# Kernel tuning notes

Hardware: AMD Instinct MI355X
Metric: run time of the kernel (lower is better)

Reference implementation:

```python
import jax, jax.numpy as jnp
import numpy as np

IGNORE_INDEX = -100


def setup_inputs() -> dict:
    key = jax.random.key(0)
    k_e, k_c, k_t = jax.random.split(key, 3)
    B, T, D, V = 1, 8192, 1024, 50257
    e = jax.random.normal(k_e, (B, T, D), dtype=jnp.float32)
    c = jax.random.normal(k_c, (V, D), dtype=jnp.float32) * (D ** -0.5)
    targets = jax.random.randint(k_t, (B, T), 0, V, dtype=jnp.int64)
    bias = jnp.zeros((V,), dtype=jnp.float32)
    return {"e": e, "c": c, "targets": targets, "bias": bias}


def _linear_cross_entropy(e, c, bias, targets, ignore_index=IGNORE_INDEX,
                          softcap=None, reduction="mean"):
    B, T, D = e.shape
    V = c.shape[0]
    ef = e.reshape(B * T, D)
    tf = targets.reshape(B * T)
    # logits: [N, V] = e @ c^T + bias
    logits = jnp.einsum("nd,vd->nv", ef, c) + bias
    if softcap is not None:
        logits = softcap * jnp.tanh(logits / softcap)
    # stable cross entropy: lse - logit[target]
    lse = jax.nn.logsumexp(logits, axis=-1)  # [N]
    safe_t = jnp.where(tf == ignore_index, 0, tf)
    tgt_logit = jnp.take_along_axis(logits, safe_t[:, None], axis=-1)[:, 0]
    nll = lse - tgt_logit  # [N]
    valid = (tf != ignore_index)
    nll = jnp.where(valid, nll, 0.0)
    if reduction == "mean":
        denom = jnp.maximum(valid.sum().astype(nll.dtype), 1.0)
        return nll.sum() / denom
    elif reduction == "sum":
        return nll.sum()
    else:  # 'none'
        return nll.reshape(B, T)


def reference(e, c, targets, bias):
    return _linear_cross_entropy(e, c, bias, targets)
```

## Files before the change

### kernel.cpp

```cpp
#include <hip/hip_runtime.h>
#include <hip/hip_bf16.h>
#include <math.h>


#define BM 128
#define BN 128
#define BKB 128

typedef int   i32x8 __attribute__((ext_vector_type(8)));
typedef float f32x4 __attribute__((ext_vector_type(4)));

__device__ __forceinline__ void load_lds16(const void* g, void* l) {
    __builtin_amdgcn_global_load_lds(
        (const __attribute__((address_space(1))) void*)g,
        (__attribute__((address_space(3))) void*)l, 16, 0, 0);
}

__device__ __forceinline__ unsigned char f2e4m3_sw(float x) {
    unsigned u = __float_as_uint(x);
    unsigned s = (u >> 24) & 0x80;
    float ax = __uint_as_float(u & 0x7fffffff);
    if (ax != ax) return (unsigned char)(s | 0x7f);
    if (ax >= 448.f) return (unsigned char)(s | 0x7e);
    if (ax < 0.0009765625f) return (unsigned char)s;
    if (ax < 0.015625f) {
        int n = (int)rintf(ax * 512.f);
        return (unsigned char)(s | n);
    }
    int e = (int)((u >> 23) & 0xff) - 127;
    unsigned m = u & 0x7fffff;
    unsigned keep = m >> 20, rest = m & 0xfffff;
    if (rest > 0x80000u || (rest == 0x80000u && (keep & 1))) keep++;
    if (keep == 8) { keep = 0; e++; if (e > 8) return (unsigned char)(s | 0x7e); }
    return (unsigned char)(s | ((e + 7) << 3) | keep);
}

__device__ __forceinline__ unsigned int pk4_fp8(float a, float b, float c, float d) {
#if __has_builtin(__builtin_amdgcn_cvt_pk_fp8_f32)
    int v = __builtin_amdgcn_cvt_pk_fp8_f32(a, b, 0, false);
    v = __builtin_amdgcn_cvt_pk_fp8_f32(c, d, v, true);
    return (unsigned int)v;
#else
    return (unsigned int)f2e4m3_sw(a) | ((unsigned int)f2e4m3_sw(b) << 8) |
           ((unsigned int)f2e4m3_sw(c) << 16) | ((unsigned int)f2e4m3_sw(d) << 24);
#endif
}

__global__ void cast_all_fp8(const float* __restrict__ e,
                             const float* __restrict__ c,
                             unsigned char* __restrict__ e_f8,
                             unsigned char* __restrict__ c_f8,
                             long ne, long ncs, long ncd) {
    long i8 = ((long)blockIdx.x * blockDim.x + threadIdx.x) * 8;
    if (i8 >= ne + ncd) return;
    const float* src;
    unsigned char* dst;
    float scale;
    bool zero = false;
    if (i8 < ne) {
        src = e + i8; dst = e_f8 + i8; scale = 1.0f;
    } else {
        long j8 = i8 - ne;
        dst = c_f8 + j8; scale = 16.0f;
        src = c + j8;
        zero = (j8 + 7 >= ncs);
    }
    uint2 o;
    if (!zero) {
        float4 v0 = *(const float4*)(src);
        float4 v1 = *(const float4*)(src + 4);
        o.x = pk4_fp8(v0.x * scale, v0.y * scale, v0.z * scale, v0.w * scale);
        o.y = pk4_fp8(v1.x * scale, v1.y * scale, v1.z * scale, v1.w * scale);
    } else {
        o.x = o.y = 0u;
    }
    *(uint2*)dst = o;
}

__global__ __launch_bounds__(256)
void gemm_lse_partial(const unsigned char* __restrict__ E,
                      const unsigned char* __restrict__ C,
                      const float* __restrict__ bias,
                      const int* __restrict__ targets,
                      float* __restrict__ row_sum,
                      float* __restrict__ tgt,
                      int N, int D, int V) {
    __shared__ unsigned char As[BM * BKB];
    __shared__ unsigned char Bs[BN * BKB];
    __shared__ float bias_s[BN];
    __shared__ int tgt_s[BM];
    __shared__ float red_s[2][BM];

    const int t = threadIdx.x;
    const int w = t >> 6;
    const int l = t & 63;
    const int quad = l >> 4;
    const int lm = l & 15;
    const int wr0 = (w >> 1) * 64;
    const int wc0 = (w & 1) * 64;

    const int mt = blockIdx.x;
    const int vt = blockIdx.y;

    if (t < BN) {
        int col = vt * BN + t;
        bias_s[t] = (col < V) ? bias[col] : -INFINITY;
    }
    if (t >= BN && t < BN + BM)
        tgt_s[t - BN] = targets[mt * BM + (t - BN)];

    const int srow = t >> 3;
    const int schunk = (t & 7) ^ (srow & 7);
    const unsigned char* ga = E + (long)(mt * BM + srow) * D + schunk * 16;
    const unsigned char* gb = C + (long)(vt * BN + srow) * D + schunk * 16;
    char* lA = (char*)As + w * 1024;
    char* lB = (char*)Bs + w * 1024;
    const long rnd = 32L * D;

    f32x4 acc[4][4] = {};
    const int sA = 127;
    const int sB = 123;

    for (int k0 = 0; k0 < D; k0 += BKB) {
#pragma unroll
        for (int ro = 0; ro < 4; ro++) {
            load_lds16(ga + k0 + ro * rnd, lA + ro * 4096);
            load_lds16(gb + k0 + ro * rnd, lB + ro * 4096);
        }
        __syncthreads();

        const int c0 = ((quad << 1) ^ (lm & 7)) << 4;
        const int c1 = c0 ^ 16;
        i32x8 a_frag[4], b_frag[4];
#pragma unroll
        for (int ti = 0; ti < 4; ti++) {
            const unsigned char* pr = As + (wr0 + ti * 16 + lm) * 128;
            int4 lo = *(const int4*)(pr + c0);
            int4 hi = *(const int4*)(pr + c1);
            a_frag[ti] = (i32x8){lo.x, lo.y, lo.z, lo.w, hi.x, hi.y, hi.z, hi.w};
        }
#pragma unroll
        for (int tj = 0; tj < 4; tj++) {
            const unsigned char* pr = Bs + (wc0 + tj * 16 + lm) * 128;
            int4 lo = *(const int4*)(pr + c0);
            int4 hi = *(const int4*)(pr + c1);
            b_frag[tj] = (i32x8){lo.x, lo.y, lo.z, lo.w, hi.x, hi.y, hi.z, hi.w};
        }
#pragma unroll
        for (int ti = 0; ti < 4; ti++)
#pragma unroll
            for (int tj = 0; tj < 4; tj++)
                acc[ti][tj] = __builtin_amdgcn_mfma_scale_f32_16x16x128_f8f6f4(
                    a_frag[ti], b_frag[tj], acc[ti][tj], 0, 0, 0, sA, 0, sB);
        __syncthreads();
    }

    float bvals[4];
#pragma unroll
    for (int tj = 0; tj < 4; tj++) bvals[tj] = bias_s[wc0 + tj * 16 + lm];

#pragma unroll
    for (int ti = 0; ti < 4; ti++) {
#pragma unroll
        for (int r = 0; r < 4; r++) {
            const int row_local = wr0 + ti * 16 + quad * 4 + r;
            const int tl = tgt_s[row_local] - vt * BN;
            float srow_ = 0.f;
#pragma unroll
            for (int tj = 0; tj < 4; tj++) {
                float v = acc[ti][tj][r] + bvals[tj];
                srow_ += __expf(v);
                if (wc0 + tj * 16 + lm == tl)
                    tgt[mt * BM + row_local] = v;
            }
#pragma unroll
            for (int off = 1; off < 16; off <<= 1)
                srow_ += __shfl_xor(srow_, off, 64);
            if (lm == 0)
                red_s[w & 1][row_local] = srow_;
        }
    }
    __syncthreads();
    if (t < BM)
        atomicAdd(&row_sum[(long)mt * BM + t], red_s[0][t] + red_s[1][t]);
}

__global__ void lse_finish(const float* __restrict__ row_sum,
                           const float* __restrict__ tgt,
                           const int* __restrict__ targets,
                           float* __restrict__ gacc, int N) {
    __shared__ float sred[8];
    int r = blockIdx.x * 256 + threadIdx.x;
    float nll = 0.f, cnt = 0.f;
    if (r < N) {
        int tg = targets[r];
        if (tg != -100) { nll = logf(row_sum[r]) - tgt[r]; cnt = 1.f; }
    }
#pragma unroll
    for (int off = 32; off; off >>= 1) {
        nll += __shfl_xor(nll, off, 64);
        cnt += __shfl_xor(cnt, off, 64);
    }
    int w = threadIdx.x >> 6, l = threadIdx.x & 63;
    if (l == 0) { sred[w] = nll; sred[4 + w] = cnt; }
    __syncthreads();
    if (threadIdx.x == 0) {
        atomicAdd(gacc, sred[0] + sred[1] + sred[2] + sred[3]);
        atomicAdd(gacc + 1, sred[4] + sred[5] + sred[6] + sred[7]);
    }
}

__global__ void final_scalar(const float* __restrict__ gacc, float* __restrict__ out) {
    out[0] = gacc[0] / fmaxf(gacc[1], 1.f);
}

extern "C" void kernel_launch(void* const* d_in, const int* in_sizes, int n_in,
                              void* d_out, int out_size, void* d_ws, size_t ws_size,
                              hipStream_t stream) {
    const float* e       = (const float*)d_in[0];
    const float* c       = (const float*)d_in[1];
    const int*   targets = (const int*)d_in[2];
    const float* bias    = (const float*)d_in[3];
    float* out = (float*)d_out;

    const int N = in_sizes[2];
    const int V = in_sizes[3];
    const int D = in_sizes[0] / N;
    const int mtiles = N / BM;
    const int vtiles = (V + BN - 1) / BN;
    const long Vpad = (long)vtiles * BN;

    char* ws = (char*)d_ws;
    size_t off = 0;
    auto alloc = [&](size_t bytes) {
        void* p = ws + off;
        off += (bytes + 255) & ~(size_t)255;
        return p;
    };
    unsigned char* e_f8 = (unsigned char*)alloc((size_t)N * D);
    unsigned char* c_f8 = (unsigned char*)alloc((size_t)Vpad * D);
    float* row_sum = (float*)alloc((size_t)N * 4);
    float* gacc    = (float*)alloc(8);
    float* tgt     = (float*)alloc((size_t)N * 4);

    hipMemsetAsync(row_sum, 0, (size_t)N * 4 + 256 + 8, stream);

    const long ne  = (long)N * D;
    const long ncs = (long)V * D;
    const long ncd = Vpad * D;
    const long tot8 = (ne + ncd) / 8;
    cast_all_fp8<<<(int)((tot8 + 255) / 256), 256, 0, stream>>>(
        e, c, e_f8, c_f8, ne, ncs, ncd);

    dim3 grid(mtiles, vtiles);
    gemm_lse_partial<<<grid, 256, 0, stream>>>(e_f8, c_f8, bias, targets,
                                               row_sum, tgt, N, D, V);

    lse_finish<<<(N + 255) / 256, 256, 0, stream>>>(row_sum, tgt, targets, gacc, N);
    final_scalar<<<1, 1, 0, stream>>>(gacc, out);
}
```

Baseline: 855.0 us.

## Use 256x256 tiles with double-buffered LDS pipeline and grid swizzle

Enlarges the GEMM tile to 256x256 with 512 threads. It double-buffers A and B in 128KB of LDS, issuing the global-to-LDS loads for the next K slice while MFMAs run on the current one, using explicit waitcnt, barriers and setprio. It also remaps block IDs with an XCD-aware swizzle over a 1D grid. The goal is to hide memory latency and raise data reuse per tile, at the cost of heavier register and LDS pressure and strict assumptions about D and the padding of N and V.

New measurement: 3.067 ms. 259% more time.

```diff
diff --git a/kernel.cpp b/kernel.cpp
--- a/kernel.cpp
+++ b/kernel.cpp
@@ -3,8 +3,8 @@
 #include <math.h>
 
 
-#define BM 128
-#define BN 128
+#define BM 256
+#define BN 256
 #define BKB 128
 
 typedef int   i32x8 __attribute__((ext_vector_type(8)));
@@ -77,112 +77,166 @@
     *(uint2*)dst = o;
 }
 
-__global__ __launch_bounds__(256)
+
+#define VM4 asm volatile("s_waitcnt vmcnt(4)" ::: "memory")
+#define VM0 asm volatile("s_waitcnt vmcnt(0)" ::: "memory")
+#define NOPW ((void)0)
+
+#define STG_A(k, h, b) do {                                                   \
+    const unsigned char* _s = gA + (size_t)(h) * 128 * D + (size_t)(k) * 128; \
+    load_lds16(_s,          lA + (b) * 32768 + (h) * 16384);                  \
+    load_lds16(_s + rowD64, lA + (b) * 32768 + (h) * 16384 + 8192);           \
+} while (0)
+
+#define STG_B(k, h, b) do {                                                   \
+    const unsigned char* _s = gB + (size_t)(h) * 128 * D + (size_t)(k) * 128; \
+    load_lds16(_s,          lB + (b) * 32768 + (h) * 16384);                  \
+    load_lds16(_s + rowD64, lB + (b) * 32768 + (h) * 16384 + 8192);           \
+} while (0)
+
+#define LDA_FRAG(dst, ti, b) do {                                             \
+    const unsigned char* _pr = ldsA + (b) * 32768 + (wr0 + (ti) * 16 + lm) * 128; \
+    int4 _lo = *(const int4*)(_pr + c0);                                      \
+    int4 _hi = *(const int4*)(_pr + c1);                                      \
+    dst = (i32x8){_lo.x, _lo.y, _lo.z, _lo.w, _hi.x, _hi.y, _hi.z, _hi.w};    \
+} while (0)
+
+#define LDB_FRAG(dst, tj, b) do {                                             \
+    const unsigned char* _pr = ldsB + (b) * 32768 + (wc0 + (tj) * 16 + lm) * 128; \
+    int4 _lo = *(const int4*)(_pr + c0);                                      \
+    int4 _hi = *(const int4*)(_pr + c1);                                      \
+    dst = (i32x8){_lo.x, _lo.y, _lo.z, _lo.w, _hi.x, _hi.y, _hi.z, _hi.w};    \
+} while (0)
+
+#define MFMA1(a, bfr, c) __builtin_amdgcn_mfma_scale_f32_16x16x128_f8f6f4(    \
+    (a), (bfr), (c), 0, 0, 0, sA, 0, sB)
+
+#define PHASE(q, b, LOADB, STAGE, WAITV) do {                                 \
+    i32x8 _a0, _a1;                                                           \
+    LDA_FRAG(_a0, 2 * (q), b);                                                \
+    LDA_FRAG(_a1, 2 * (q) + 1, b);                                            \
+    if (LOADB) {                                                              \
+        LDB_FRAG(bf0, 0, b); LDB_FRAG(bf1, 1, b);                             \
+        LDB_FRAG(bf2, 2, b); LDB_FRAG(bf3, 3, b);                             \
+    }                                                                         \
+    STAGE;                                                                    \
+    WAITV;                                                                    \
+    __builtin_amdgcn_s_barrier();                                             \
+    asm volatile("s_waitcnt lgkmcnt(0)" ::: "memory");                        \
+    __builtin_amdgcn_sched_barrier(0);                                        \
+    __builtin_amdgcn_s_setprio(1);                                            \
+    acc[2 * (q)][0]     = MFMA1(_a0, bf0, acc[2 * (q)][0]);                   \
+    acc[2 * (q)][1]     = MFMA1(_a0, bf1, acc[2 * (q)][1]);                   \
+    acc[2 * (q)][2]     = MFMA1(_a0, bf2, acc[2 * (q)][2]);                   \
+    acc[2 * (q)][3]     = MFMA1(_a0, bf3, acc[2 * (q)][3]);                   \
+    acc[2 * (q) + 1][0] = MFMA1(_a1, bf0, acc[2 * (q) + 1][0]);               \
+    acc[2 * (q) + 1][1] = MFMA1(_a1, bf1, acc[2 * (q) + 1][1]);               \
+    acc[2 * (q) + 1][2] = MFMA1(_a1, bf2, acc[2 * (q) + 1][2]);               \
+    acc[2 * (q) + 1][3] = MFMA1(_a1, bf3, acc[2 * (q) + 1][3]);               \
+    __builtin_amdgcn_s_setprio(0);                                            \
+    __builtin_amdgcn_sched_barrier(0);                                        \
+    __builtin_amdgcn_s_barrier();                                             \
+    asm volatile("" ::: "memory");                                            \
+} while (0)
+
+__global__ __launch_bounds__(512, 2)
 void gemm_lse_partial(const unsigned char* __restrict__ E,
                       const unsigned char* __restrict__ C,
                       const float* __restrict__ bias,
                       const int* __restrict__ targets,
                       float* __restrict__ row_sum,
                       float* __restrict__ tgt,
-                      int N, int D, int V) {
-    __shared__ unsigned char As[BM * BKB];
-    __shared__ unsigned char Bs[BN * BKB];
-    __shared__ float bias_s[BN];
-    __shared__ int tgt_s[BM];
-    __shared__ float red_s[2][BM];
-
-    const int t = threadIdx.x;
-    const int w = t >> 6;
-    const int l = t & 63;
+                      int N, int D, int V, int mtiles) {
+    __shared__ unsigned char smem[131072];
+    unsigned char* ldsA = smem;
+    unsigned char* ldsB = smem + 65536;
+
+    const int t_ = threadIdx.x;
+    const int w  = t_ >> 6;
+    const int l  = t_ & 63;
     const int quad = l >> 4;
     const int lm = l & 15;
-    const int wr0 = (w >> 1) * 64;
-    const int wc0 = (w & 1) * 64;
-
-    const int mt = blockIdx.x;
-    const int vt = blockIdx.y;
-
-    if (t < BN) {
-        int col = vt * BN + t;
-        bias_s[t] = (col < V) ? bias[col] : -INFINITY;
-    }
-    if (t >= BN && t < BN + BM)
-        tgt_s[t - BN] = targets[mt * BM + (t - BN)];
-
-    const int srow = t >> 3;
-    const int schunk = (t & 7) ^ (srow & 7);
-    const unsigned char* ga = E + (long)(mt * BM + srow) * D + schunk * 16;
-    const unsigned char* gb = C + (long)(vt * BN + srow) * D + schunk * 16;
-    char* lA = (char*)As + w * 1024;
-    char* lB = (char*)Bs + w * 1024;
-    const long rnd = 32L * D;
-
-    f32x4 acc[4][4] = {};
+    const int wr0 = (w >> 2) * 128;
+    const int wc0 = (w & 3) * 64;
+    const int c0 = ((quad << 1) ^ (lm & 7)) << 4;
+    const int c1 = c0 ^ 16;
+
+    const int nwg = (int)gridDim.x;
+    int swz;
+    if (nwg & 7) swz = (int)blockIdx.x;
+    else         swz = ((int)blockIdx.x & 7) * (nwg >> 3) + ((int)blockIdx.x >> 3);
+    const int mt = swz % mtiles;
+    const int vt = swz / mtiles;
+    const int m0 = mt * BM;
+    const int v0 = vt * BN;
+
+    const int sr = t_ >> 3;
+    const int gc = (t_ & 7) ^ (sr & 7);
+    const unsigned char* gA = E + (size_t)(m0 + sr) * D + gc * 16;
+    const unsigned char* gB = C + (size_t)(v0 + sr) * D + gc * 16;
+    unsigned char* lA = ldsA + w * 1024;
+    unsigned char* lB = ldsB + w * 1024;
+    const size_t rowD64 = (size_t)64 * D;
+
+    f32x4 acc[8][4] = {};
+    i32x8 bf0, bf1, bf2, bf3;
     const int sA = 127;
     const int sB = 123;
-
-    for (int k0 = 0; k0 < D; k0 += BKB) {
-#pragma unroll
-        for (int ro = 0; ro < 4; ro++) {
-            load_lds16(ga + k0 + ro * rnd, lA + ro * 4096);
-            load_lds16(gb + k0 + ro * rnd, lB + ro * 4096);
+    const int KT  = D / BKB;
+    const int NIT = KT / 2;
+
+    STG_A(0, 0, 0); STG_A(0, 1, 0);
+    STG_B(0, 0, 0); STG_B(0, 1, 0);
+    STG_B(1, 0, 1); STG_B(1, 1, 1);
+    VM4;
+    __builtin_amdgcn_s_barrier();
+    asm volatile("" ::: "memory");
+
+    for (int t = 0; t < NIT; ++t) {
+        const int k0 = 2 * t;
+        const bool full = (t < NIT - 1);
+        PHASE(0, 0, 1, STG_A(k0 + 1, 0, 1), NOPW);
+        PHASE(1, 0, 0, STG_A(k0 + 1, 1, 1), NOPW);
+        PHASE(2, 0, 0, if (full) STG_B(k0 + 2, 0, 0), NOPW);
+        PHASE(3, 0, 0, if (full) STG_B(k0 + 2, 1, 0), if (full) VM4; else VM0);
+        PHASE(0, 1, 1, if (full) STG_A(k0 + 2, 0, 0), NOPW);
+        PHASE(1, 1, 0, if (full) STG_A(k0 + 2, 1, 0), NOPW);
+        PHASE(2, 1, 0, if (full) STG_B(k0 + 3, 0, 1), NOPW);
+        PHASE(3, 1, 0, if (full) STG_B(k0 + 3, 1, 1), if (full) VM4; else VM0);
+    }
+
+    __syncthreads();
+    float* red = (float*)smem;
+
+    float bv[4];
+#pragma unroll
+    for (int tj = 0; tj < 4; tj++) {
+        int col = v0 + wc0 + tj * 16 + lm;
+        bv[tj] = (col < V) ? bias[col] : -INFINITY;
+    }
+#pragma unroll
+    for (int ti = 0; ti < 8; ti++) {
+#pragma unroll
+        for (int r = 0; r < 4; r++) {
+            const int rl = wr0 + ti * 16 + quad * 4 + r;
+            const int tl = targets[m0 + rl] - v0 - wc0;
+            float s = 0.f;
+#pragma unroll
+            for (int tj = 0; tj < 4; tj++) {
+                float v = acc[ti][tj][r] + bv[tj];
+                s += __expf(v);
+                if (tj * 16 + lm == tl) tgt[m0 + rl] = v;
+            }
+#pragma unroll
+            for (int off = 1; off < 16; off <<= 1)
+                s += __shfl_xor(s, off, 64);
+            if (lm == 0) red[(w & 3) * 256 + rl] = s;
         }
-        __syncthreads();
-
-        const int c0 = ((quad << 1) ^ (lm & 7)) << 4;
-        const int c1 = c0 ^ 16;
-        i32x8 a_frag[4], b_frag[4];
-#pragma unroll
-        for (int ti = 0; ti < 4; ti++) {
-            const unsigned char* pr = As + (wr0 + ti * 16 + lm) * 128;
-            int4 lo = *(const int4*)(pr + c0);
-            int4 hi = *(const int4*)(pr + c1);
-            a_frag[ti] = (i32x8){lo.x, lo.y, lo.z, lo.w, hi.x, hi.y, hi.z, hi.w};
-        }
-#pragma unroll
-        for (int tj = 0; tj < 4; tj++) {
-            const unsigned char* pr = Bs + (wc0 + tj * 16 + lm) * 128;
-            int4 lo = *(const int4*)(pr + c0);
-            int4 hi = *(const int4*)(pr + c1);
-            b_frag[tj] = (i32x8){lo.x, lo.y, lo.z, lo.w, hi.x, hi.y, hi.z, hi.w};
-        }
-#pragma unroll
-        for (int ti = 0; ti < 4; ti++)
-#pragma unroll
-            for (int tj = 0; tj < 4; tj++)
-                acc[ti][tj] = __builtin_amdgcn_mfma_scale_f32_16x16x128_f8f6f4(
-                    a_frag[ti], b_frag[tj], acc[ti][tj], 0, 0, 0, sA, 0, sB);
-        __syncthreads();
-    }
-
-    float bvals[4];
-#pragma unroll
-    for (int tj = 0; tj < 4; tj++) bvals[tj] = bias_s[wc0 + tj * 16 + lm];
-
-#pragma unroll
-    for (int ti = 0; ti < 4; ti++) {
-#pragma unroll
-        for (int r = 0; r < 4; r++) {
-            const int row_local = wr0 + ti * 16 + quad * 4 + r;
-            const int tl = tgt_s[row_local] - vt * BN;
-            float srow_ = 0.f;
-#pragma unroll
-            for (int tj = 0; tj < 4; tj++) {
-                float v = acc[ti][tj][r] + bvals[tj];
-                srow_ += __expf(v);
-                if (wc0 + tj * 16 + lm == tl)
-                    tgt[mt * BM + row_local] = v;
-            }
-#pragma unroll
-            for (int off = 1; off < 16; off <<= 1)
-                srow_ += __shfl_xor(srow_, off, 64);
-            if (lm == 0)
-                red_s[w & 1][row_local] = srow_;
-        }
     }
     __syncthreads();
-    if (t < BM)
-        atomicAdd(&row_sum[(long)mt * BM + t], red_s[0][t] + red_s[1][t]);
+    if (t_ < 256)
+        atomicAdd(&row_sum[m0 + t_],
+                  red[t_] + red[256 + t_] + red[512 + t_] + red[768 + t_]);
 }
 
 __global__ void lse_finish(const float* __restrict__ row_sum,
@@ -252,9 +306,9 @@
     cast_all_fp8<<<(int)((tot8 + 255) / 256), 256, 0, stream>>>(
         e, c, e_f8, c_f8, ne, ncs, ncd);
 
-    dim3 grid(mtiles, vtiles);
-    gemm_lse_partial<<<grid, 256, 0, stream>>>(e_f8, c_f8, bias, targets,
-                                               row_sum, tgt, N, D, V);
+    const int nblk = mtiles * vtiles;
+    gemm_lse_partial<<<nblk, 512, 0, stream>>>(e_f8, c_f8, bias, targets,
+                                               row_sum, tgt, N, D, V, mtiles);
 
     lse_finish<<<(N + 255) / 256, 256, 0, stream>>>(row_sum, tgt, targets, gacc, N);
     final_scalar<<<1, 1, 0, stream>>>(gacc, out);
```
